# Kernel tuning notes

Hardware: AMD Instinct MI355X
Metric: run time of the kernel (lower is better)

Reference implementation:

```python
import jax, jax.numpy as jnp
import numpy as np

N = 50000          # nodes
E = 1600000        # edges (before self-loops)
DIN = 128
HEADS = (8, 8, 4)
FEATS = (16, 16, 16)
NEG_SLOPE = 0.2


def setup_inputs() -> dict:
    key = jax.random.key(0)
    ks = jax.random.split(key, 2 + 4 * 3)
    inp = {
        "X": jax.random.normal(ks[0], (N, DIN), dtype=jnp.float32),
        "A": jax.random.randint(ks[1], (2, E), 0, N, dtype=jnp.int32),
    }
    in_dims = [DIN, HEADS[0] * FEATS[0], HEADS[1] * FEATS[1]]
    k = 2
    for i, (h, f) in enumerate(zip(HEADS, FEATS)):
        din = in_dims[i]
        concat = i + 1 < len(HEADS)
        inp[f"W{i+1}"] = jax.random.normal(ks[k], (din, h * f), dtype=jnp.float32) / np.float32(np.sqrt(din)); k += 1
        inp[f"as{i+1}"] = jax.random.normal(ks[k], (h, f), dtype=jnp.float32) * 0.1; k += 1
        inp[f"ad{i+1}"] = jax.random.normal(ks[k], (h, f), dtype=jnp.float32) * 0.1; k += 1
        inp[f"b{i+1}"] = jnp.zeros((h * f if concat else f,), dtype=jnp.float32); k += 1
    return inp


def _gat_conv(x, src, dst, W, a_src, a_dst, b, concat):
    # PyG-style GATConv (eval mode, self-loops already in src/dst)
    H, F = a_src.shape
    h = (x @ W).reshape(-1, H, F)                     # [N, H, F]
    e = jax.nn.leaky_relu((h * a_src).sum(-1)[src] + (h * a_dst).sum(-1)[dst], NEG_SLOPE)  # [Etot, H]
    m = jax.ops.segment_max(e, dst, num_segments=N)   # segment softmax over dst neighborhoods
    ex = jnp.exp(e - m[dst])
    s = jax.ops.segment_sum(ex, dst, num_segments=N)
    alpha = ex / (s[dst] + 1e-16)                     # [Etot, H]
    out = jax.ops.segment_sum(h[src] * alpha[:, :, None], dst, num_segments=N)  # [N, H, F]
    out = out.reshape(N, H * F) if concat else out.mean(axis=1)
    return out + b


def reference(X, A, W1, as1, ad1, b1, W2, as2, ad2, b2, W3, as3, ad3, b3):
    loops = jnp.arange(N, dtype=A.dtype)              # GATConv default add_self_loops=True
    src = jnp.concatenate([A[0], loops])
    dst = jnp.concatenate([A[1], loops])
    x = jax.nn.relu(_gat_conv(X, src, dst, W1, as1, ad1, b1, True))
    x = jax.nn.relu(_gat_conv(x, src, dst, W2, as2, ad2, b2, True))
    return _gat_conv(x, src, dst, W3, as3, ad3, b3, False)
```

## Files before the change

kernel.cpp:

```cpp
#include <hip/hip_runtime.h>
#include <hip/hip_bf16.h>

#define NN 50000
#define EE 1600000
#define DIN 128

#define BKT_SHIFT 6
#define NB ((NN + 63) >> 6)
#define BSLACK 2688
#define CHUNK 4096

typedef _Float16 half_t;
typedef __attribute__((ext_vector_type(2))) _Float16 half2_t;
typedef __attribute__((ext_vector_type(4))) _Float16 half4_t;
typedef __attribute__((ext_vector_type(8))) _Float16 half8_t;
typedef __attribute__((ext_vector_type(4))) float float4_t;

__device__ __forceinline__ void split_write(half_t* __restrict__ bh, half_t* __restrict__ bl,
                                            int idx, float v) {
    half_t h = (half_t)v;
    bh[idx] = h;
    bl[idx] = (half_t)(v - (float)h);
}

__device__ __forceinline__ void build_bt(const float* __restrict__ W,
                                         const float* __restrict__ as,
                                         const float* __restrict__ ad,
                                         half_t* __restrict__ Bh, half_t* __restrict__ Bl,
                                         int elem, int NCOL, int H) {
    int r = elem >> 7, k = elem & 127;
    float v;
    if (r < NCOL) {
        v = W[k * NCOL + r];
    } else {
        int j = r - NCOL;
        v = 0.f;
        if (j < 8) {
            if (j < H) {
                float s = 0.f;
#pragma unroll
                for (int f = 0; f < 16; ++f) s += W[k * NCOL + j * 16 + f] * as[j * 16 + f];
                v = s;
            }
        } else {
            int hh = j - 8;
            if (hh < H) {
                float s = 0.f;
#pragma unroll
                for (int f = 0; f < 16; ++f) s += W[k * NCOL + hh * 16 + f] * ad[hh * 16 + f];
                v = s;
            }
        }
    }
    split_write(Bh, Bl, r * 128 + k, v);
}

#define T1 (144 * 128)
#define T3 (80 * 128)
__global__ __launch_bounds__(256) void prep_kernel(
    const float* __restrict__ W1, const float* __restrict__ W2, const float* __restrict__ W3,
    const float* __restrict__ as1, const float* __restrict__ ad1,
    const float* __restrict__ as2, const float* __restrict__ ad2,
    const float* __restrict__ as3, const float* __restrict__ ad3,
    half_t* __restrict__ B1h, half_t* __restrict__ B1l,
    half_t* __restrict__ B2h, half_t* __restrict__ B2l,
    half_t* __restrict__ B3h, half_t* __restrict__ B3l,
    int* __restrict__ gcursor) {
    int id = blockIdx.x * 256 + threadIdx.x;
    if (id < T1) {
        build_bt(W1, as1, ad1, B1h, B1l, id, 128, 8);
    } else if (id < 2 * T1) {
        build_bt(W2, as2, ad2, B2h, B2l, id - T1, 128, 8);
    } else if (id < 2 * T1 + T3) {
        build_bt(W3, as3, ad3, B3h, B3l, id - 2 * T1, 64, 4);
    } else {
        int i = id - (2 * T1 + T3);
        if (i < NB) gcursor[i] = 0;
    }
}

__global__ __launch_bounds__(256) void bin_kernel(const int* __restrict__ A,
                                                  int* __restrict__ gcursor,
                                                  int* __restrict__ binned, int e, int n) {
    __shared__ int lcount[NB];
    __shared__ int lbase[NB];
    int chunk0 = blockIdx.x * CHUNK;
    int cend = chunk0 + CHUNK;
    if (cend > e + n) cend = e + n;
    for (int i = threadIdx.x; i < NB; i += 256) lcount[i] = 0;
    __syncthreads();
    int sreg[16], dreg[16];
#pragma unroll
    for (int l = 0; l < 16; ++l) {
        int i = chunk0 + l * 256 + threadIdx.x;
        if (i < cend) {
            if (i < e) { sreg[l] = A[i]; dreg[l] = A[e + i]; }
            else       { sreg[l] = dreg[l] = i - e; }
            atomicAdd(&lcount[dreg[l] >> BKT_SHIFT], 1);
        } else {
            dreg[l] = -1;
        }
    }
    __syncthreads();
    for (int b = threadIdx.x; b < NB; b += 256) {
        int c = lcount[b];
        lbase[b] = c ? atomicAdd(&gcursor[b], c) : 0;
        lcount[b] = 0;
    }
    __syncthreads();
#pragma unroll
    for (int l = 0; l < 16; ++l) {
        if (dreg[l] >= 0) {
            int bkt = dreg[l] >> BKT_SHIFT;
            int pos = lbase[bkt] + atomicAdd(&lcount[bkt], 1);
            if (pos < BSLACK)
                binned[(size_t)bkt * BSLACK + pos] = (sreg[l] << 6) | (dreg[l] & 63);
        }
    }
}

__global__ __launch_bounds__(256) void fine_scatter(const int* __restrict__ binned,
                                                    const int* __restrict__ gcursor,
                                                    int* __restrict__ begE,
                                                    int* __restrict__ endE,
                                                    int* __restrict__ csr) {
    __shared__ int lc[64];
    __shared__ int scur[64];
    int b = blockIdx.x;
    int node0 = b << BKT_SHIFT;
    int cnt = gcursor[b];
    if (cnt > BSLACK) cnt = BSLACK;
    const int* bp = binned + (size_t)b * BSLACK;
    if (threadIdx.x < 64) lc[threadIdx.x] = 0;
    __syncthreads();
    for (int j = threadIdx.x; j < cnt; j += 256) atomicAdd(&lc[bp[j] & 63], 1);
    __syncthreads();
    if (threadIdx.x < 64) {
        int lane = threadIdx.x;
        int c = lc[lane];
        int v = c;
#pragma unroll
        for (int off = 1; off < 64; off <<= 1) {
            int u = __shfl_up(v, off, 64);
            if (lane >= off) v += u;
        }
        int begin = b * BSLACK + v - c;
        scur[lane] = begin;
        int node = node0 + lane;
        if (node < NN) {
            begE[node] = begin;
            endE[node] = begin + c;
        }
    }
    __syncthreads();
    for (int j = threadIdx.x; j < cnt; j += 256) {
        int v = bp[j];
        int pos = atomicAdd(&scur[v & 63], 1);
        csr[pos] = v >> 6;
    }
}

template <int NTC, int H, int AMODE, bool CSL>
__global__ __launch_bounds__(256) void gemm_mfma(
    const float* __restrict__ X32,
    const half_t* __restrict__ Ah, const half_t* __restrict__ Al,
    const half_t* __restrict__ Bth, const half_t* __restrict__ Btl,
    half_t* __restrict__ C16, float* __restrict__ ss, float* __restrict__ ds, int M) {
    constexpr int NCOL = NTC * 16;
    constexpr int NR = NTC + 1;
    constexpr int NCHUNK = NR * 256;
    __shared__ __align__(16) half_t Bs[2][NR * 2048];
    int tid = threadIdx.x;
    int w = tid >> 6, lane = tid & 63;
    int m = lane & 15, q = lane >> 4;
    int row0 = blockIdx.x * 64 + w * 16;

    for (int P = tid; P < NCHUNK; P += 256) {
        int nt = P >> 8, k0 = (P >> 6) & 3, qq = (P >> 4) & 3, mm = P & 15;
        int src = (nt * 16 + mm) * 128 + qq * 8 + k0 * 32;
        *(half8_t*)&Bs[0][(size_t)P * 8] = *(const half8_t*)&Bth[src];
        *(half8_t*)&Bs[1][(size_t)P * 8] = *(const half8_t*)&Btl[src];
    }

    int ar = row0 + m;
    if (ar >= M) ar = M - 1;
    half8_t ahf[4], alf[4];
    if constexpr (AMODE == 0) {
        const float* px = X32 + (size_t)ar * 128 + q * 8;
#pragma unroll
        for (int k0 = 0; k0 < 4; ++k0) {
            float4 u0 = *(const float4*)(px + k0 * 32);
            float4 u1 = *(const float4*)(px + k0 * 32 + 4);
            float uv[8] = {u0.x, u0.y, u0.z, u0.w, u1.x, u1.y, u1.z, u1.w};
#pragma unroll
            for (int j = 0; j < 8; ++j) {
                half_t h = (half_t)uv[j];
                ahf[k0][j] = h;
                alf[k0][j] = (half_t)(uv[j] - (float)h);
            }
        }
    } else {
#pragma unroll
        for (int k0 = 0; k0 < 4; ++k0) {
            size_t base = ((size_t)k0 * M + ar) * 32 + q * 8;
            ahf[k0] = *(const half8_t*)(Ah + base);
            alf[k0] = *(const half8_t*)(Al + base);
        }
    }

    __syncthreads();

    float4_t acc[NR];
#pragma unroll
    for (int nt = 0; nt < NR; ++nt) {
        acc[nt][0] = 0.f; acc[nt][1] = 0.f; acc[nt][2] = 0.f; acc[nt][3] = 0.f;
    }

#pragma unroll
    for (int nt = 0; nt < NR; ++nt) {
#pragma unroll
        for (int k0 = 0; k0 < 4; ++k0) {
            half8_t bh = *(const half8_t*)&Bs[0][(size_t)((nt * 4 + k0) * 64 + lane) * 8];
            half8_t bl = *(const half8_t*)&Bs[1][(size_t)((nt * 4 + k0) * 64 + lane) * 8];
            acc[nt] = __builtin_amdgcn_mfma_f32_16x16x32_f16(ahf[k0], bh, acc[nt], 0, 0, 0);
            acc[nt] = __builtin_amdgcn_mfma_f32_16x16x32_f16(ahf[k0], bl, acc[nt], 0, 0, 0);
            acc[nt] = __builtin_amdgcn_mfma_f32_16x16x32_f16(alf[k0], bh, acc[nt], 0, 0, 0);
        }
    }

#pragma unroll
    for (int r = 0; r < 4; ++r) {
        int grow = row0 + q * 4 + r;
        if (grow < M) {
            float v = acc[NTC][r];
            if constexpr (CSL) {
                if (m < H) ss[(((size_t)(m >> 1)) * M + grow) * 2 + (m & 1)] = v;
                else if (m >= 8 && m < 8 + H) ds[(size_t)grow * H + (m - 8)] = v;
            } else {
                if (m < H) ss[(size_t)grow * H + m] = v;
                else if (m >= 8 && m < 8 + H) ds[(size_t)grow * H + (m - 8)] = v;
            }
        }
    }

    __syncthreads();
    half_t* cs = (half_t*)Bs;
#pragma unroll
    for (int nt = 0; nt < NTC; ++nt)
#pragma unroll
        for (int r = 0; r < 4; ++r)
            cs[(size_t)(w * 16 + q * 4 + r) * NCOL + nt * 16 + m] = (half_t)acc[nt][r];
    if constexpr (CSL) {
        int sl = lane >> 4, rr = (lane >> 2) & 3, c = lane & 3;
#pragma unroll
        for (int pass = 0; pass < 4; ++pass) {
            int r = pass * 4 + rr;
            int grow = row0 + r;
            half8_t v = *(const half8_t*)&cs[(size_t)(w * 16 + r) * NCOL + sl * 32 + c * 8];
            if (grow < M) *(half8_t*)(C16 + ((size_t)sl * M + grow) * 32 + c * 8) = v;
        }
    } else {
        constexpr int LPR = NCOL / 8;
        constexpr int RPP = 64 / LPR;
        constexpr int NP = 16 / RPP;
        int rid = lane / LPR, cid = lane % LPR;
#pragma unroll
        for (int p = 0; p < NP; ++p) {
            int r = p * RPP + rid;
            int grow = row0 + r;
            half8_t v = *(const half8_t*)&cs[(size_t)(w * 16 + r) * NCOL + cid * 8];
            if (grow < M) *(half8_t*)(C16 + (size_t)grow * NCOL + cid * 8) = v;
        }
    }
}

template <bool RELU>
__global__ __launch_bounds__(256) void aggregate_x(
    const half_t* __restrict__ hS, const float* __restrict__ ssS,
    const float* __restrict__ dsc_arr,
    const int* __restrict__ csr, const int* __restrict__ begE, const int* __restrict__ endE,
    const float* __restrict__ bias, half_t* __restrict__ outh, half_t* __restrict__ outl,
    int n) {
    constexpr int H = 8, SW = 32;
    int b = blockIdx.x;
    int s = b & 3;
    int d = (b >> 2) * 4 + (threadIdx.x >> 6);
    if (d >= n) return;
    int lane = threadIdx.x & 63;
    int g = lane >> 3, fl = lane & 7;
    int f0 = s * SW + fl * 4;
    int hh = f0 >> 4;
    int sc = fl >> 2;
    float dsc = dsc_arr[(size_t)d * H + hh];
    const float* ssp = ssS + (size_t)s * n * 2;
    const half_t* hp = hS + (size_t)s * n * SW;
    int begin = begE[d], end = endE[d];

    float ssum = 0.f, a0 = 0.f, a1 = 0.f, a2 = 0.f, a3 = 0.f;
    int j = begin + g;
    for (; j + 8 < end; j += 16) {
        int u0 = csr[j], u1 = csr[j + 8];
        float e0 = ssp[u0 * 2 + sc], e1 = ssp[u1 * 2 + sc];
        half4_t t0 = *(const half4_t*)(hp + (size_t)u0 * SW + fl * 4);
        half4_t t1 = *(const half4_t*)(hp + (size_t)u1 * SW + fl * 4);
        e0 += dsc; e0 = (e0 > 0.f) ? e0 : 0.2f * e0;
        e1 += dsc; e1 = (e1 > 0.f) ? e1 : 0.2f * e1;
        float x0 = __expf(e0), x1 = __expf(e1);
        ssum += x0 + x1;
        a0 = fmaf(x0, (float)t0[0], a0); a0 = fmaf(x1, (float)t1[0], a0);
        a1 = fmaf(x0, (float)t0[1], a1); a1 = fmaf(x1, (float)t1[1], a1);
        a2 = fmaf(x0, (float)t0[2], a2); a2 = fmaf(x1, (float)t1[2], a2);
        a3 = fmaf(x0, (float)t0[3], a3); a3 = fmaf(x1, (float)t1[3], a3);
    }
    for (; j < end; j += 8) {
        int u = csr[j];
        float e = ssp[u * 2 + sc] + dsc;
        e = (e > 0.f) ? e : 0.2f * e;
        half4_t t = *(const half4_t*)(hp + (size_t)u * SW + fl * 4);
        float x = __expf(e);
        ssum += x;
        a0 = fmaf(x, (float)t[0], a0);
        a1 = fmaf(x, (float)t[1], a1);
        a2 = fmaf(x, (float)t[2], a2);
        a3 = fmaf(x, (float)t[3], a3);
    }

    ssum += __shfl_xor(ssum, 8, 64);
    ssum += __shfl_xor(ssum, 16, 64);
    ssum += __shfl_xor(ssum, 32, 64);
    a0 += __shfl_xor(a0, 8, 64); a0 += __shfl_xor(a0, 16, 64); a0 += __shfl_xor(a0, 32, 64);
    a1 += __shfl_xor(a1, 8, 64); a1 += __shfl_xor(a1, 16, 64); a1 += __shfl_xor(a1, 32, 64);
    a2 += __shfl_xor(a2, 8, 64); a2 += __shfl_xor(a2, 16, 64); a2 += __shfl_xor(a2, 32, 64);
    a3 += __shfl_xor(a3, 8, 64); a3 += __shfl_xor(a3, 16, 64); a3 += __shfl_xor(a3, 32, 64);

    if (lane < 8) {
        float inv = 1.f / (ssum + 1e-16f);
        float v0 = a0 * inv + bias[f0 + 0];
        float v1 = a1 * inv + bias[f0 + 1];
        float v2 = a2 * inv + bias[f0 + 2];
        float v3 = a3 * inv + bias[f0 + 3];
        if (RELU) {
            v0 = fmaxf(v0, 0.f); v1 = fmaxf(v1, 0.f);
            v2 = fmaxf(v2, 0.f); v3 = fmaxf(v3, 0.f);
        }
        half4_t hh4, ll4;
        hh4[0] = (half_t)v0; ll4[0] = (half_t)(v0 - (float)hh4[0]);
        hh4[1] = (half_t)v1; ll4[1] = (half_t)(v1 - (float)hh4[1]);
        hh4[2] = (half_t)v2; ll4[2] = (half_t)(v2 - (float)hh4[2]);
        hh4[3] = (half_t)v3; ll4[3] = (half_t)(v3 - (float)hh4[3]);
        size_t o = ((size_t)s * n + d) * SW + fl * 4;
        *(half4_t*)(outh + o) = hh4;
        *(half4_t*)(outl + o) = ll4;
    }
}

__global__ __launch_bounds__(256) void aggregate_l3(
    const half_t* __restrict__ h, const float* __restrict__ ss, const float* __restrict__ dsc_arr,
    const int* __restrict__ csr, const int* __restrict__ begE, const int* __restrict__ endE,
    const float* __restrict__ bias, float* __restrict__ out, int n) {
    constexpr int H = 4, F = 16, HF = 64, FPL = 4;
    int wave = blockIdx.x * (blockDim.x >> 6) + (threadIdx.x >> 6);
    int lane = threadIdx.x & 63;
    if (wave >= n) return;
    int q = lane >> 4, ql = lane & 15;
    int hf = ql * FPL;
    int hh = hf / F;
    float dsc = dsc_arr[wave * H + hh];
    int begin = begE[wave], end = endE[wave];

    float ssum = 0.f;
    float acc[FPL] = {};

    int j = begin + q;
    for (; j + 12 < end; j += 16) {
        int s0 = csr[j], s1 = csr[j + 4], s2 = csr[j + 8], s3 = csr[j + 12];
        float e0 = ss[s0 * H + hh], e1 = ss[s1 * H + hh];
        float e2 = ss[s2 * H + hh], e3 = ss[s3 * H + hh];
        const half_t* p0 = h + (size_t)s0 * HF + hf;
        const half_t* p1 = h + (size_t)s1 * HF + hf;
        const half_t* p2 = h + (size_t)s2 * HF + hf;
        const half_t* p3 = h + (size_t)s3 * HF + hf;
        e0 += dsc; e0 = (e0 > 0.f) ? e0 : 0.2f * e0;
        e1 += dsc; e1 = (e1 > 0.f) ? e1 : 0.2f * e1;
        e2 += dsc; e2 = (e2 > 0.f) ? e2 : 0.2f * e2;
        e3 += dsc; e3 = (e3 > 0.f) ? e3 : 0.2f * e3;
        float x0 = __expf(e0), x1 = __expf(e1), x2 = __expf(e2), x3 = __expf(e3);
        ssum += (x0 + x1) + (x2 + x3);
        half4_t t0 = *(const half4_t*)p0, t1 = *(const half4_t*)p1;
        half4_t t2 = *(const half4_t*)p2, t3 = *(const half4_t*)p3;
#pragma unroll
        for (int k = 0; k < 4; ++k) {
            acc[k] = fmaf(x0, (float)t0[k], acc[k]);
            acc[k] = fmaf(x1, (float)t1[k], acc[k]);
            acc[k] = fmaf(x2, (float)t2[k], acc[k]);
            acc[k] = fmaf(x3, (float)t3[k], acc[k]);
        }
    }
    for (; j < end; j += 4) {
        int s = csr[j];
        float e = ss[s * H + hh] + dsc;
        e = (e > 0.f) ? e : 0.2f * e;
        float x = __expf(e);
        ssum += x;
        half4_t t = *(const half4_t*)(h + (size_t)s * HF + hf);
#pragma unroll
        for (int k = 0; k < 4; ++k) acc[k] = fmaf(x, (float)t[k], acc[k]);
    }

    ssum += __shfl_xor(ssum, 16, 64);
    ssum += __shfl_xor(ssum, 32, 64);
#pragma unroll
    for (int k = 0; k < FPL; ++k) {
        acc[k] += __shfl_xor(acc[k], 16, 64);
        acc[k] += __shfl_xor(acc[k], 32, 64);
    }

    float inv = 1.f / (ssum + 1e-16f);
    float val[FPL];
#pragma unroll
    for (int k = 0; k < FPL; ++k) {
        val[k] = acc[k] * inv;
        val[k] += __shfl_xor(val[k], 4, 64);
        val[k] += __shfl_xor(val[k], 8, 64);
    }
    if (lane < 4) {
        float v0 = val[0] * 0.25f + bias[lane * 4 + 0];
        float v1 = val[1] * 0.25f + bias[lane * 4 + 1];
        float v2 = val[2] * 0.25f + bias[lane * 4 + 2];
        float v3 = val[3] * 0.25f + bias[lane * 4 + 3];
        *(float4*)(out + (size_t)wave * F + lane * 4) = make_float4(v0, v1, v2, v3);
    }
}

extern "C" void kernel_launch(void* const* d_in, const int* in_sizes, int n_in,
                              void* d_out, int out_size, void* d_ws, size_t ws_size,
                              hipStream_t stream) {
    const float* X  = (const float*)d_in[0];
    const int*   A  = (const int*)d_in[1];
    const float* W1 = (const float*)d_in[2];
    const float* as1 = (const float*)d_in[3];
    const float* ad1 = (const float*)d_in[4];
    const float* b1  = (const float*)d_in[5];
    const float* W2 = (const float*)d_in[6];
    const float* as2 = (const float*)d_in[7];
    const float* ad2 = (const float*)d_in[8];
    const float* b2  = (const float*)d_in[9];
    const float* W3 = (const float*)d_in[10];
    const float* as3 = (const float*)d_in[11];
    const float* ad3 = (const float*)d_in[12];
    const float* b3  = (const float*)d_in[13];

    const int N = NN, E = EE;
    const int Etot = E + N;

    char* p = (char*)d_ws;
    auto take = [&](size_t bytes) {
        char* r = p;
        p += (bytes + 255) & ~(size_t)255;
        return (void*)r;
    };
    half_t* C16   = (half_t*)take((size_t)N * 128 * 2);
    half_t* Ph    = (half_t*)take((size_t)N * 128 * 2);
    half_t* Pl    = (half_t*)take((size_t)N * 128 * 2);
    float* ssb    = (float*)take((size_t)N * 8 * 4);
    float* dsb    = (float*)take((size_t)N * 8 * 4);
    int* begE     = (int*)take((size_t)N * 4);
    int* endE     = (int*)take((size_t)N * 4);
    int* gcursor  = (int*)take((size_t)NB * 4);
    int* csr      = (int*)take((size_t)NB * BSLACK * 4);
    half_t* B1h   = (half_t*)take(144 * 128 * 2);
    half_t* B1l   = (half_t*)take(144 * 128 * 2);
    half_t* B2h   = (half_t*)take(144 * 128 * 2);
    half_t* B2l   = (half_t*)take(144 * 128 * 2);
    half_t* B3h   = (half_t*)take(80 * 128 * 2);
    half_t* B3l   = (half_t*)take(80 * 128 * 2);
    int* binned   = (int*)Ph;

    const int prepTotal = 2 * T1 + T3 + NB;
    prep_kernel<<<(prepTotal + 255) / 256, 256, 0, stream>>>(
        W1, W2, W3, as1, ad1, as2, ad2, as3, ad3,
        B1h, B1l, B2h, B2l, B3h, B3l, gcursor);
    bin_kernel<<<(Etot + CHUNK - 1) / CHUNK, 256, 0, stream>>>(A, gcursor, binned, E, N);
    fine_scatter<<<NB, 256, 0, stream>>>(binned, gcursor, begE, endE, csr);

    const int gemmRows = (N + 63) / 64;
    const int aggXBlocks = ((N + 3) / 4) * 4;
    const int aggBlocks = (N + 3) / 4;

    gemm_mfma<8, 8, 0, true><<<gemmRows, 256, 0, stream>>>(X, nullptr, nullptr,
                                                           B1h, B1l, C16, ssb, dsb, N);
    aggregate_x<true><<<aggXBlocks, 256, 0, stream>>>(
        C16, ssb, dsb, csr, begE, endE, b1, Ph, Pl, N);

    gemm_mfma<8, 8, 1, true><<<gemmRows, 256, 0, stream>>>(nullptr, Ph, Pl,
                                                           B2h, B2l, C16, ssb, dsb, N);
    aggregate_x<true><<<aggXBlocks, 256, 0, stream>>>(
        C16, ssb, dsb, csr, begE, endE, b2, Ph, Pl, N);

    gemm_mfma<4, 4, 1, false><<<gemmRows, 256, 0, stream>>>(nullptr, Ph, Pl,
                                                            B3h, B3l, C16, ssb, dsb, N);
    aggregate_l3<<<aggBlocks, 256, 0, stream>>>(
        C16, ssb, dsb, csr, begE, endE, b3, (float*)d_out, N);
}
```

Measured before the change: 406.7 us.

## Precompute edge attention weights once and compact CSR with global bucket scan

Adds a separate alpha kernel that computes exp(leaky_relu) attention weights per edge and head and the inverse softmax denominators. Each feature-slice aggregation pass then reads these instead of recomputing scores four times per edge. A single-block prefix scan over bucket counts lets the CSR be stored compacted rather than with per-bucket slack, which improves locality. The aggregation is widened to 8 halves per lane. The trade-off is an extra kernel launch and a large per-edge alpha buffer (about 53 MB) written and reread each layer. The score layout produced by the GEMM is also simplified.

```diff
diff --git a/kernel.cpp b/kernel.cpp
--- a/kernel.cpp
+++ b/kernel.cpp
@@ -4,6 +4,7 @@
 #define NN 50000
 #define EE 1600000
 #define DIN 128
+#define ETOT (EE + NN)
 
 #define BKT_SHIFT 6
 #define NB ((NN + 63) >> 6)
@@ -119,8 +120,25 @@
     }
 }
 
+__global__ void scan_nb(const int* __restrict__ gcursor, int* __restrict__ bbase) {
+    __shared__ int s[1024];
+    int t = threadIdx.x;
+    int c = (t < NB) ? gcursor[t] : 0;
+    if (c > BSLACK) c = BSLACK;
+    s[t] = c;
+    __syncthreads();
+    for (int off = 1; off < 1024; off <<= 1) {
+        int u = (t >= off) ? s[t - off] : 0;
+        __syncthreads();
+        s[t] += u;
+        __syncthreads();
+    }
+    if (t < NB) bbase[t] = s[t] - c;
+}
+
 __global__ __launch_bounds__(256) void fine_scatter(const int* __restrict__ binned,
                                                     const int* __restrict__ gcursor,
+                                                    const int* __restrict__ bbase,
                                                     int* __restrict__ begE,
                                                     int* __restrict__ endE,
                                                     int* __restrict__ csr) {
@@ -144,7 +162,7 @@
             int u = __shfl_up(v, off, 64);
             if (lane >= off) v += u;
         }
-        int begin = b * BSLACK + v - c;
+        int begin = bbase[b] + v - c;
         scur[lane] = begin;
         int node = node0 + lane;
         if (node < NN) {
@@ -233,13 +251,8 @@
         int grow = row0 + q * 4 + r;
         if (grow < M) {
             float v = acc[NTC][r];
-            if constexpr (CSL) {
-                if (m < H) ss[(((size_t)(m >> 1)) * M + grow) * 2 + (m & 1)] = v;
-                else if (m >= 8 && m < 8 + H) ds[(size_t)grow * H + (m - 8)] = v;
-            } else {
-                if (m < H) ss[(size_t)grow * H + m] = v;
-                else if (m >= 8 && m < 8 + H) ds[(size_t)grow * H + (m - 8)] = v;
-            }
+            if (m < H) ss[(size_t)grow * H + m] = v;
+            else if (m >= 8 && m < 8 + H) ds[(size_t)grow * H + (m - 8)] = v;
         }
     }
 
@@ -274,83 +287,108 @@
     }
 }
 
+__global__ __launch_bounds__(256) void alpha_kernel(
+    const float* __restrict__ ss, const float* __restrict__ ds,
+    const int* __restrict__ csr, const int* __restrict__ begE, const int* __restrict__ endE,
+    float* __restrict__ alphaS, float* __restrict__ invS, int n) {
+    int d = blockIdx.x * 4 + (threadIdx.x >> 6);
+    if (d >= n) return;
+    int lane = threadIdx.x & 63;
+    int g = lane >> 3, hh = lane & 7;
+    float dscv = ds[(size_t)d * 8 + hh];
+    int begin = begE[d], end = endE[d];
+    float* ap = alphaS + (size_t)(hh >> 1) * ETOT * 2 + (hh & 1);
+    float ssum = 0.f;
+    int j = begin + g;
+    for (; j + 8 < end; j += 16) {
+        int s0 = csr[j], s1 = csr[j + 8];
+        float e0 = ss[s0 * 8 + hh] + dscv;
+        float e1 = ss[s1 * 8 + hh] + dscv;
+        e0 = (e0 > 0.f) ? e0 : 0.2f * e0;
+        e1 = (e1 > 0.f) ? e1 : 0.2f * e1;
+        float x0 = __expf(e0), x1 = __expf(e1);
+        ssum += x0 + x1;
+        ap[(size_t)j * 2] = x0;
+        ap[(size_t)(j + 8) * 2] = x1;
+    }
+    for (; j < end; j += 8) {
+        int s = csr[j];
+        float e = ss[s * 8 + hh] + dscv;
+        e = (e > 0.f) ? e : 0.2f * e;
+        float x = __expf(e);
+        ssum += x;
+        ap[(size_t)j * 2] = x;
+    }
+    ssum += __shfl_xor(ssum, 8, 64);
+    ssum += __shfl_xor(ssum, 16, 64);
+    ssum += __shfl_xor(ssum, 32, 64);
+    if (g == 0) invS[(size_t)d * 8 + hh] = 1.f / (ssum + 1e-16f);
+}
+
 template <bool RELU>
-__global__ __launch_bounds__(256) void aggregate_x(
-    const half_t* __restrict__ hS, const float* __restrict__ ssS,
-    const float* __restrict__ dsc_arr,
+__global__ __launch_bounds__(256) void aggregate_b(
+    const half_t* __restrict__ hS, const float* __restrict__ alphaS,
+    const float* __restrict__ invS,
     const int* __restrict__ csr, const int* __restrict__ begE, const int* __restrict__ endE,
     const float* __restrict__ bias, half_t* __restrict__ outh, half_t* __restrict__ outl,
     int n) {
-    constexpr int H = 8, SW = 32;
+    constexpr int SW = 32;
     int b = blockIdx.x;
     int s = b & 3;
     int d = (b >> 2) * 4 + (threadIdx.x >> 6);
     if (d >= n) return;
     int lane = threadIdx.x & 63;
-    int g = lane >> 3, fl = lane & 7;
-    int f0 = s * SW + fl * 4;
-    int hh = f0 >> 4;
-    int sc = fl >> 2;
-    float dsc = dsc_arr[(size_t)d * H + hh];
-    const float* ssp = ssS + (size_t)s * n * 2;
+    int g = lane >> 2, fl = lane & 3;
+    int f0 = s * SW + fl * 8;
+    int sc = fl >> 1;
     const half_t* hp = hS + (size_t)s * n * SW;
+    const float* ap = alphaS + (size_t)s * ETOT * 2 + sc;
+    float inv = invS[(size_t)d * 8 + s * 2 + sc];
     int begin = begE[d], end = endE[d];
 
-    float ssum = 0.f, a0 = 0.f, a1 = 0.f, a2 = 0.f, a3 = 0.f;
+    float acc[8] = {};
     int j = begin + g;
-    for (; j + 8 < end; j += 16) {
-        int u0 = csr[j], u1 = csr[j + 8];
-        float e0 = ssp[u0 * 2 + sc], e1 = ssp[u1 * 2 + sc];
-        half4_t t0 = *(const half4_t*)(hp + (size_t)u0 * SW + fl * 4);
-        half4_t t1 = *(const half4_t*)(hp + (size_t)u1 * SW + fl * 4);
-        e0 += dsc; e0 = (e0 > 0.f) ? e0 : 0.2f * e0;
-        e1 += dsc; e1 = (e1 > 0.f) ? e1 : 0.2f * e1;
-        float x0 = __expf(e0), x1 = __expf(e1);
-        ssum += x0 + x1;
-        a0 = fmaf(x0, (float)t0[0], a0); a0 = fmaf(x1, (float)t1[0], a0);
-        a1 = fmaf(x0, (float)t0[1], a1); a1 = fmaf(x1, (float)t1[1], a1);
-        a2 = fmaf(x0, (float)t0[2], a2); a2 = fmaf(x1, (float)t1[2], a2);
-        a3 = fmaf(x0, (float)t0[3], a3); a3 = fmaf(x1, (float)t1[3], a3);
-    }
-    for (; j < end; j += 8) {
+    for (; j + 16 < end; j += 32) {
+        int u0 = csr[j], u1 = csr[j + 16];
+        float x0 = ap[(size_t)j * 2];
+        float x1 = ap[(size_t)(j + 16) * 2];
+        half8_t t0 = *(const half8_t*)(hp + (size_t)u0 * SW + fl * 8);
+        half8_t t1 = *(const half8_t*)(hp + (size_t)u1 * SW + fl * 8);
+#pragma unroll
+        for (int k = 0; k < 8; ++k) {
+            acc[k] = fmaf(x0, (float)t0[k], acc[k]);
+            acc[k] = fmaf(x1, (float)t1[k], acc[k]);
+        }
+    }
+    for (; j < end; j += 16) {
         int u = csr[j];
-        float e = ssp[u * 2 + sc] + dsc;
-        e = (e > 0.f) ? e : 0.2f * e;
-        half4_t t = *(const half4_t*)(hp + (size_t)u * SW + fl * 4);
-        float x = __expf(e);
-        ssum += x;
-        a0 = fmaf(x, (float)t[0], a0);
-        a1 = fmaf(x, (float)t[1], a1);
-        a2 = fmaf(x, (float)t[2], a2);
-        a3 = fmaf(x, (float)t[3], a3);
-    }
-
-    ssum += __shfl_xor(ssum, 8, 64);
-    ssum += __shfl_xor(ssum, 16, 64);
-    ssum += __shfl_xor(ssum, 32, 64);
-    a0 += __shfl_xor(a0, 8, 64); a0 += __shfl_xor(a0, 16, 64); a0 += __shfl_xor(a0, 32, 64);
-    a1 += __shfl_xor(a1, 8, 64); a1 += __shfl_xor(a1, 16, 64); a1 += __shfl_xor(a1, 32, 64);
-    a2 += __shfl_xor(a2, 8, 64); a2 += __shfl_xor(a2, 16, 64); a2 += __shfl_xor(a2, 32, 64);
-    a3 += __shfl_xor(a3, 8, 64); a3 += __shfl_xor(a3, 16, 64); a3 += __shfl_xor(a3, 32, 64);
-
-    if (lane < 8) {
-        float inv = 1.f / (ssum + 1e-16f);
-        float v0 = a0 * inv + bias[f0 + 0];
-        float v1 = a1 * inv + bias[f0 + 1];
-        float v2 = a2 * inv + bias[f0 + 2];
-        float v3 = a3 * inv + bias[f0 + 3];
-        if (RELU) {
-            v0 = fmaxf(v0, 0.f); v1 = fmaxf(v1, 0.f);
-            v2 = fmaxf(v2, 0.f); v3 = fmaxf(v3, 0.f);
-        }
-        half4_t hh4, ll4;
-        hh4[0] = (half_t)v0; ll4[0] = (half_t)(v0 - (float)hh4[0]);
-        hh4[1] = (half_t)v1; ll4[1] = (half_t)(v1 - (float)hh4[1]);
-        hh4[2] = (half_t)v2; ll4[2] = (half_t)(v2 - (float)hh4[2]);
-        hh4[3] = (half_t)v3; ll4[3] = (half_t)(v3 - (float)hh4[3]);
-        size_t o = ((size_t)s * n + d) * SW + fl * 4;
-        *(half4_t*)(outh + o) = hh4;
-        *(half4_t*)(outl + o) = ll4;
+        float x = ap[(size_t)j * 2];
+        half8_t t = *(const half8_t*)(hp + (size_t)u * SW + fl * 8);
+#pragma unroll
+        for (int k = 0; k < 8; ++k) acc[k] = fmaf(x, (float)t[k], acc[k]);
+    }
+
+#pragma unroll
+    for (int k = 0; k < 8; ++k) {
+        acc[k] += __shfl_xor(acc[k], 4, 64);
+        acc[k] += __shfl_xor(acc[k], 8, 64);
+        acc[k] += __shfl_xor(acc[k], 16, 64);
+        acc[k] += __shfl_xor(acc[k], 32, 64);
+    }
+
+    if (lane < 4) {
+        half8_t hh8, ll8;
+#pragma unroll
+        for (int k = 0; k < 8; ++k) {
+            float v = acc[k] * inv + bias[f0 + k];
+            if (RELU) v = fmaxf(v, 0.f);
+            half_t h = (half_t)v;
+            hh8[k] = h;
+            ll8[k] = (half_t)(v - (float)h);
+        }
+        size_t o = ((size_t)s * n + d) * SW + fl * 8;
+        *(half8_t*)(outh + o) = hh8;
+        *(half8_t*)(outl + o) = ll8;
     }
 }
 
@@ -462,12 +500,15 @@
     half_t* C16   = (half_t*)take((size_t)N * 128 * 2);
     half_t* Ph    = (half_t*)take((size_t)N * 128 * 2);
     half_t* Pl    = (half_t*)take((size_t)N * 128 * 2);
+    float* alphaS = (float*)take((size_t)4 * ETOT * 2 * 4);
+    float* invS   = (float*)take((size_t)N * 8 * 4);
     float* ssb    = (float*)take((size_t)N * 8 * 4);
     float* dsb    = (float*)take((size_t)N * 8 * 4);
     int* begE     = (int*)take((size_t)N * 4);
     int* endE     = (int*)take((size_t)N * 4);
     int* gcursor  = (int*)take((size_t)NB * 4);
-    int* csr      = (int*)take((size_t)NB * BSLACK * 4);
+    int* bbase    = (int*)take((size_t)NB * 4);
+    int* csr      = (int*)take((size_t)Etot * 4);
     half_t* B1h   = (half_t*)take(144 * 128 * 2);
     half_t* B1l   = (half_t*)take(144 * 128 * 2);
     half_t* B2h   = (half_t*)take(144 * 128 * 2);
@@ -481,24 +522,27 @@
         W1, W2, W3, as1, ad1, as2, ad2, as3, ad3,
         B1h, B1l, B2h, B2l, B3h, B3l, gcursor);
     bin_kernel<<<(Etot + CHUNK - 1) / CHUNK, 256, 0, stream>>>(A, gcursor, binned, E, N);
-    fine_scatter<<<NB, 256, 0, stream>>>(binned, gcursor, begE, endE, csr);
+    scan_nb<<<1, 1024, 0, stream>>>(gcursor, bbase);
+    fine_scatter<<<NB, 256, 0, stream>>>(binned, gcursor, bbase, begE, endE, csr);
 
     const int gemmRows = (N + 63) / 64;
-    const int aggXBlocks = ((N + 3) / 4) * 4;
-    const int aggBlocks = (N + 3) / 4;
+    const int nodeBlocks = (N + 3) / 4;
+    const int aggXBlocks = nodeBlocks * 4;
 
     gemm_mfma<8, 8, 0, true><<<gemmRows, 256, 0, stream>>>(X, nullptr, nullptr,
                                                            B1h, B1l, C16, ssb, dsb, N);
-    aggregate_x<true><<<aggXBlocks, 256, 0, stream>>>(
-        C16, ssb, dsb, csr, begE, endE, b1, Ph, Pl, N);
+    alpha_kernel<<<nodeBlocks, 256, 0, stream>>>(ssb, dsb, csr, begE, endE, alphaS, invS, N);
+    aggregate_b<true><<<aggXBlocks, 256, 0, stream>>>(
+        C16, alphaS, invS, csr, begE, endE, b1, Ph, Pl, N);
 
     gemm_mfma<8, 8, 1, true><<<gemmRows, 256, 0, stream>>>(nullptr, Ph, Pl,
                                                            B2h, B2l, C16, ssb, dsb, N);
-    aggregate_x<true><<<aggXBlocks, 256, 0, stream>>>(
-        C16, ssb, dsb, csr, begE, endE, b2, Ph, Pl, N);
+    alpha_kernel<<<nodeBlocks, 256, 0, stream>>>(ssb, dsb, csr, begE, endE, alphaS, invS, N);
+    aggregate_b<true><<<aggXBlocks, 256, 0, stream>>>(
+        C16, alphaS, invS, csr, begE, endE, b2, Ph, Pl, N);
 
     gemm_mfma<4, 4, 1, false><<<gemmRows, 256, 0, stream>>>(nullptr, Ph, Pl,
                                                             B3h, B3l, C16, ssb, dsb, N);
-    aggregate_l3<<<aggBlocks, 256, 0, stream>>>(
+    aggregate_l3<<<nodeBlocks, 256, 0, stream>>>(
         C16, ssb, dsb, csr, begE, endE, b3, (float*)d_out, N);
 }
```

Result: slower. 442.2 us (+8.7%).
